# Kernel optimization log

Measured on AMD Instinct MI355X. Metric: run time of the kernel, lower is better.

Reference implementation:

```python
import jax, jax.numpy as jnp
import numpy as np
import math

D_MODEL = 1024
NUM_HEADS = 16
D_K = D_MODEL // NUM_HEADS
THETA = 10000.0
CONTEXT_LENGTH = 2048


def _rope_tables(seq_len):
    # freqs: [d_k/2]
    powers = jnp.arange(0, D_K, 2, dtype=jnp.float32) / D_K
    freqs = 1.0 / (THETA ** powers)
    t = jnp.arange(seq_len, dtype=jnp.float32)
    fm = jnp.outer(t, freqs)  # [s, d_k/2]
    return jnp.cos(fm), jnp.sin(fm)


def _apply_rope(x, cos, sin):
    # x: [b, h, s, d_k]; cos/sin: [s, d_k/2] broadcast to [1,1,s,d_k/2]
    c = cos[None, None, :, :].astype(x.dtype)
    s_ = sin[None, None, :, :].astype(x.dtype)
    xe = x[..., 0::2]
    xo = x[..., 1::2]
    oe = xe * c - xo * s_
    oo = xe * s_ + xo * c
    # interleave even/odd back
    out = jnp.stack([oe, oo], axis=-1).reshape(x.shape)
    return out


def setup_inputs() -> dict:
    key = jax.random.key(0)
    ks = jax.random.split(key, 5)
    b, s = 4, 2048
    std = (2.0 / (D_MODEL + D_MODEL)) ** 0.5
    x = jax.random.normal(ks[0], (b, s, D_MODEL), dtype=jnp.float32)
    Wq = jax.random.normal(ks[1], (D_MODEL, D_MODEL), dtype=jnp.float32) * std
    Wk = jax.random.normal(ks[2], (D_MODEL, D_MODEL), dtype=jnp.float32) * std
    Wv = jax.random.normal(ks[3], (D_MODEL, D_MODEL), dtype=jnp.float32) * std
    Wo = jax.random.normal(ks[4], (D_MODEL, D_MODEL), dtype=jnp.float32) * std
    return {"x": x, "Wq": Wq, "Wk": Wk, "Wv": Wv, "Wo": Wo}


def reference(x, Wq, Wk, Wv, Wo):
    b, s, d = x.shape
    h, dk = NUM_HEADS, D_K
    # projections: Linear applies x @ W.T via einsum('...i,oi->...o')
    def proj(W):
        y = jnp.einsum('bsi,oi->bso', x, W)
        return y.reshape(b, s, h, dk).transpose(0, 2, 1, 3)  # [b,h,s,dk]
    q, k, v = proj(Wq), proj(Wk), proj(Wv)
    cos, sin = _rope_tables(s)
    q = _apply_rope(q, cos, sin)
    k = _apply_rope(k, cos, sin)
    scores = jnp.einsum('bhnd,bhmd->bhnm', q, k) / math.sqrt(dk)
    causal = jnp.tril(jnp.ones((s, s), dtype=bool))
    scores = jnp.where(causal, scores, -jnp.inf)
    probs = jax.nn.softmax(scores, axis=-1)
    attn = jnp.einsum('bhnm,bhmd->bhnd', probs, v)
    attn = attn.transpose(0, 2, 1, 3).reshape(b, s, d)  # [b,s,d_model]
    return jnp.einsum('bsi,oi->bso', attn, Wo)
```

## Files before the change

### kernel.cpp

```cpp
#include <hip/hip_runtime.h>
#include <hip/hip_bf16.h>
#include <math.h>

typedef __attribute__((ext_vector_type(4))) float f32x4;
typedef __attribute__((ext_vector_type(8))) short s16x8;

#define LDSP(p) ((__attribute__((address_space(3))) void*)(p))
#define GLBP(p) ((const __attribute__((address_space(1))) void*)(p))

__device__ __forceinline__ unsigned short f2b(float f) {
  unsigned u = __builtin_bit_cast(unsigned, f);
  u += 0x7FFFu + ((u >> 16) & 1u);
  return (unsigned short)(u >> 16);
}
__device__ __forceinline__ float b2f(unsigned short h) {
  unsigned u = ((unsigned)h) << 16;
  return __builtin_bit_cast(float, u);
}

__global__ void cvt_f2b_kernel(const float* __restrict__ src, unsigned short* __restrict__ dst, int n8) {
  int i = blockIdx.x * blockDim.x + threadIdx.x;
  if (i >= n8) return;
  const float4* s = (const float4*)src;
  float4 a = s[2 * i], b = s[2 * i + 1];
  s16x8 o;
  o[0] = (short)f2b(a.x); o[1] = (short)f2b(a.y); o[2] = (short)f2b(a.z); o[3] = (short)f2b(a.w);
  o[4] = (short)f2b(b.x); o[5] = (short)f2b(b.y); o[6] = (short)f2b(b.z); o[7] = (short)f2b(b.w);
  ((s16x8*)dst)[i] = o;
}

__global__ void rope_table_kernel(float* __restrict__ cosT, float* __restrict__ sinT) {
  int idx = blockIdx.x * 256 + threadIdx.x;
  int s = idx >> 5, j = idx & 31;
  float freq = (float)(1.0 / pow(10000.0, (double)(2 * j) / 64.0));
  float fm = (float)s * freq;
  cosT[idx] = cosf(fm);
  sinT[idx] = sinf(fm);
}

__global__ void rope_apply_kernel(unsigned short* __restrict__ qk, const float* __restrict__ cosT,
                                  const float* __restrict__ sinT, float scale) {
  int i = blockIdx.x * 256 + threadIdx.x;
  int e = i * 8;
  int s = (e >> 6) & 2047;
  int jb = (e & 63) >> 1;
  s16x8 v = ((const s16x8*)qk)[i];
  float4 c = *(const float4*)(cosT + s * 32 + jb);
  float4 sn = *(const float4*)(sinT + s * 32 + jb);
  float cc[4] = {c.x, c.y, c.z, c.w}, ss[4] = {sn.x, sn.y, sn.z, sn.w};
  s16x8 o;
#pragma unroll
  for (int p = 0; p < 4; ++p) {
    float e_ = b2f((unsigned short)v[2 * p]);
    float o_ = b2f((unsigned short)v[2 * p + 1]);
    o[2 * p]     = (short)f2b((e_ * cc[p] - o_ * ss[p]) * scale);
    o[2 * p + 1] = (short)f2b((e_ * ss[p] + o_ * cc[p]) * scale);
  }
  ((s16x8*)qk)[i] = o;
}

template <int EPI>
__global__ void gemm_bt_kernel(const unsigned short* __restrict__ A, const unsigned short* __restrict__ B,
                               float* __restrict__ Cf, unsigned short* __restrict__ Cq,
                               unsigned short* __restrict__ Ck, unsigned short* __restrict__ Cv,
                               int M, int N, int K) {
  __shared__ __align__(16) unsigned short As[128 * 64];
  __shared__ __align__(16) unsigned short Bs[128 * 64];
  const int t = threadIdx.x;
  const int lane = t & 63, wave = t >> 6;
  const int wm = wave >> 1, wn = wave & 1;
  const int g = lane >> 4, q = lane & 15;
  const int m0 = blockIdx.x * 128, n0 = blockIdx.y * 128;
  const int srow = t >> 3;
  const int scol = (t & 7) << 4;
  f32x4 acc[4][4] = {};
  const int nkt = K >> 6;
  for (int kt = 0; kt < nkt; ++kt) {
    __syncthreads();
#pragma unroll
    for (int it = 0; it < 4; ++it) {
      int row = it * 32 + srow;
      int cg = scol ^ ((row & 7) << 4);
      const char* ga = (const char*)A + ((size_t)(m0 + row) * K + (kt << 6)) * 2 + cg;
      __builtin_amdgcn_global_load_lds(GLBP(ga), LDSP((char*)As + it * 4096 + wave * 1024), 16, 0, 0);
      const char* gb = (const char*)B + ((size_t)(n0 + row) * K + (kt << 6)) * 2 + cg;
      __builtin_amdgcn_global_load_lds(GLBP(gb), LDSP((char*)Bs + it * 4096 + wave * 1024), 16, 0, 0);
    }
    asm volatile("s_waitcnt vmcnt(0)" ::: "memory");
    __syncthreads();
#pragma unroll
    for (int kk = 0; kk < 2; ++kk) {
      const int colB = ((kk << 6) + (g << 4)) ^ ((q & 7) << 4);
      s16x8 af[4], bf[4];
#pragma unroll
      for (int x = 0; x < 4; ++x) {
        af[x] = *(const s16x8*)(As + (wm * 64 + x * 16 + q) * 64 + (colB >> 1));
        bf[x] = *(const s16x8*)(Bs + (wn * 64 + x * 16 + q) * 64 + (colB >> 1));
      }
#pragma unroll
      for (int mi = 0; mi < 4; ++mi)
#pragma unroll
        for (int ni = 0; ni < 4; ++ni)
          acc[mi][ni] = __builtin_amdgcn_mfma_f32_16x16x32_bf16(af[mi], bf[ni], acc[mi][ni], 0, 0, 0);
    }
  }
  if (EPI == 0) {
#pragma unroll
    for (int mi = 0; mi < 4; ++mi)
#pragma unroll
      for (int r = 0; r < 4; ++r) {
        int m = m0 + wm * 64 + mi * 16 + g * 4 + r;
#pragma unroll
        for (int ni = 0; ni < 4; ++ni) {
          int n = n0 + wn * 64 + ni * 16 + q;
          Cf[(size_t)m * N + n] = acc[mi][ni][r];
        }
      }
  } else {
    unsigned short* dst = (n0 < 1024) ? Cq : (n0 < 2048 ? Ck : Cv);
    const int obase = n0 & 1023;
#pragma unroll
    for (int mi = 0; mi < 4; ++mi)
#pragma unroll
      for (int r = 0; r < 4; ++r) {
        int m = m0 + wm * 64 + mi * 16 + g * 4 + r;
        int bb = m >> 11, s = m & 2047;
#pragma unroll
        for (int ni = 0; ni < 4; ++ni) {
          int o = obase + wn * 64 + ni * 16 + q;
          int hh = o >> 6, d = o & 63;
          dst[(((size_t)bb * 16 + hh) * 2048 + s) * 64 + d] = f2b(acc[mi][ni][r]);
        }
      }
  }
}

__global__ void attn_kernel(const unsigned short* __restrict__ Q, const unsigned short* __restrict__ K,
                            const unsigned short* __restrict__ V, unsigned short* __restrict__ O) {
  __shared__ __align__(16) unsigned short Ks[64 * 64];
  __shared__ __align__(16) unsigned short Vt[64 * 72];
  __shared__ __align__(16) unsigned short Ps[4 * 16 * 72];
  const int t = threadIdx.x;
  const int lane = t & 63, w = t >> 6;
  const int g = lane >> 4, q = lane & 15;
  const int bh = blockIdx.x;
  const int qt = 31 - (int)blockIdx.y;
  const size_t hoff = (size_t)bh * 2048 * 64;
  s16x8 qa[2];
  {
    const unsigned short* qp = Q + hoff + (size_t)(qt * 64 + w * 16 + q) * 64 + g * 8;
    qa[0] = *(const s16x8*)qp;
    qa[1] = *(const s16x8*)(qp + 32);
  }
  f32x4 accO[4] = {};
  float mrun[4] = {-3e38f, -3e38f, -3e38f, -3e38f};
  float lrun[4] = {0.f, 0.f, 0.f, 0.f};
  const int srow = t >> 3;
  const int scol = (t & 7) << 4;
  unsigned short* pw = Ps + w * (16 * 72);
  for (int tk = 0; tk <= qt; ++tk) {
    __syncthreads();
    const char* kb = (const char*)(K + hoff + (size_t)tk * 4096);
#pragma unroll
    for (int it = 0; it < 2; ++it) {
      int row = it * 32 + srow;
      int cg = scol ^ ((row & 7) << 4);
      __builtin_amdgcn_global_load_lds(GLBP(kb + row * 128 + cg), LDSP((char*)Ks + it * 4096 + w * 1024), 16, 0, 0);
    }
    {
      const unsigned short* vb = V + hoff + (size_t)tk * 4096;
#pragma unroll
      for (int p = 0; p < 2; ++p) {
        int d0 = w * 8 + p * 32;
        s16x8 vv = *(const s16x8*)(vb + lane * 64 + d0);
#pragma unroll
        for (int j = 0; j < 8; ++j) Vt[(d0 + j) * 72 + lane] = (unsigned short)vv[j];
      }
    }
    asm volatile("s_waitcnt vmcnt(0)" ::: "memory");
    __syncthreads();
    f32x4 accS[4] = {};
#pragma unroll
    for (int kk = 0; kk < 2; ++kk) {
      const int colB = ((kk << 6) + (g << 4)) ^ ((q & 7) << 4);
      s16x8 kf[4];
#pragma unroll
      for (int ni = 0; ni < 4; ++ni)
        kf[ni] = *(const s16x8*)(Ks + (ni * 16 + q) * 64 + (colB >> 1));
#pragma unroll
      for (int ni = 0; ni < 4; ++ni)
        accS[ni] = __builtin_amdgcn_mfma_f32_16x16x32_bf16(qa[kk], kf[ni], accS[ni], 0, 0, 0);
    }
    if (tk == qt) {
#pragma unroll
      for (int ni = 0; ni < 4; ++ni)
#pragma unroll
        for (int r = 0; r < 4; ++r) {
          int qrow = w * 16 + g * 4 + r;
          int kvc = ni * 16 + q;
          if (kvc > qrow) accS[ni][r] = -3e38f;
        }
    }
    float alph[4];
#pragma unroll
    for (int r = 0; r < 4; ++r) {
      float mx = fmaxf(fmaxf(accS[0][r], accS[1][r]), fmaxf(accS[2][r], accS[3][r]));
      mx = fmaxf(mx, __shfl_xor(mx, 1));
      mx = fmaxf(mx, __shfl_xor(mx, 2));
      mx = fmaxf(mx, __shfl_xor(mx, 4));
      mx = fmaxf(mx, __shfl_xor(mx, 8));
      float mnew = fmaxf(mrun[r], mx);
      float sum = 0.f;
#pragma unroll
      for (int ni = 0; ni < 4; ++ni) {
        float p = __expf(accS[ni][r] - mnew);
        accS[ni][r] = p;
        sum += p;
      }
      sum += __shfl_xor(sum, 1);
      sum += __shfl_xor(sum, 2);
      sum += __shfl_xor(sum, 4);
      sum += __shfl_xor(sum, 8);
      float alpha = __expf(mrun[r] - mnew);
      lrun[r] = lrun[r] * alpha + sum;
      mrun[r] = mnew;
      alph[r] = alpha;
    }
#pragma unroll
    for (int ni = 0; ni < 4; ++ni)
#pragma unroll
      for (int r = 0; r < 4; ++r) accO[ni][r] *= alph[r];
#pragma unroll
    for (int ni = 0; ni < 4; ++ni)
#pragma unroll
      for (int r = 0; r < 4; ++r)
        pw[(g * 4 + r) * 72 + ni * 16 + q] = f2b(accS[ni][r]);
#pragma unroll
    for (int kk = 0; kk < 2; ++kk) {
      s16x8 pa = *(const s16x8*)(pw + q * 72 + kk * 32 + g * 8);
#pragma unroll
      for (int ni = 0; ni < 4; ++ni) {
        s16x8 vf = *(const s16x8*)(Vt + (ni * 16 + q) * 72 + kk * 32 + g * 8);
        accO[ni] = __builtin_amdgcn_mfma_f32_16x16x32_bf16(pa, vf, accO[ni], 0, 0, 0);
      }
    }
  }
  const int bb = bh >> 4, hh = bh & 15;
#pragma unroll
  for (int ni = 0; ni < 4; ++ni)
#pragma unroll
    for (int r = 0; r < 4; ++r) {
      int s = qt * 64 + w * 16 + g * 4 + r;
      O[((size_t)(bb * 2048 + s)) * 1024 + hh * 64 + ni * 16 + q] = f2b(accO[ni][r] / lrun[r]);
    }
}

extern "C" void kernel_launch(void* const* d_in, const int* in_sizes, int n_in,
                              void* d_out, int out_size, void* d_ws, size_t ws_size,
                              hipStream_t stream) {
  const float* x  = (const float*)d_in[0];
  const float* Wq = (const float*)d_in[1];
  const float* Wk = (const float*)d_in[2];
  const float* Wv = (const float*)d_in[3];
  const float* Wo = (const float*)d_in[4];
  char* ws = (char*)d_ws;
  unsigned short* xb   = (unsigned short*)(ws);
  unsigned short* wqkv = (unsigned short*)(ws + 16777216);
  unsigned short* wo   = (unsigned short*)(ws + 23068672);
  unsigned short* qb   = (unsigned short*)(ws + 25165824);
  unsigned short* kb   = (unsigned short*)(ws + 41943040);
  unsigned short* vb   = (unsigned short*)(ws + 58720256);
  unsigned short* ab   = (unsigned short*)(ws + 75497472);
  float* cosT = (float*)(ws + 92274688);
  float* sinT = (float*)(ws + 92536832);

  cvt_f2b_kernel<<<4096, 256, 0, stream>>>(x, xb, 1048576);
  cvt_f2b_kernel<<<512, 256, 0, stream>>>(Wq, wqkv, 131072);
  cvt_f2b_kernel<<<512, 256, 0, stream>>>(Wk, wqkv + 1048576, 131072);
  cvt_f2b_kernel<<<512, 256, 0, stream>>>(Wv, wqkv + 2097152, 131072);
  cvt_f2b_kernel<<<512, 256, 0, stream>>>(Wo, wo, 131072);
  rope_table_kernel<<<256, 256, 0, stream>>>(cosT, sinT);
  gemm_bt_kernel<1><<<dim3(64, 24), 256, 0, stream>>>(xb, wqkv, nullptr, qb, kb, vb, 8192, 3072, 1024);
  rope_apply_kernel<<<4096, 256, 0, stream>>>(qb, cosT, sinT, 0.125f);
  rope_apply_kernel<<<4096, 256, 0, stream>>>(kb, cosT, sinT, 1.0f);
  attn_kernel<<<dim3(64, 32), 256, 0, stream>>>(qb, kb, vb, ab);
  gemm_bt_kernel<0><<<dim3(64, 8), 256, 0, stream>>>(ab, wo, (float*)d_out, nullptr, nullptr, nullptr, 8192, 1024, 1024);
}
```

Baseline: 304.4 us.

## Rewrite attention with 32x32 MFMA, 128-row query tiles, register-resident P

```diff
diff --git a/kernel.cpp b/kernel.cpp
--- a/kernel.cpp
+++ b/kernel.cpp
@@ -3,7 +3,9 @@
 #include <math.h>
 
 typedef __attribute__((ext_vector_type(4))) float f32x4;
+typedef __attribute__((ext_vector_type(16))) float f32x16;
 typedef __attribute__((ext_vector_type(8))) short s16x8;
+typedef __attribute__((ext_vector_type(4))) unsigned u32x4;
 
 #define LDSP(p) ((__attribute__((address_space(3))) void*)(p))
 #define GLBP(p) ((const __attribute__((address_space(1))) void*)(p))
@@ -16,6 +18,11 @@
 __device__ __forceinline__ float b2f(unsigned short h) {
   unsigned u = ((unsigned)h) << 16;
   return __builtin_bit_cast(float, u);
+}
+__device__ __forceinline__ unsigned cvtpk_bf16(float lo, float hi) {
+  unsigned r;
+  asm("v_cvt_pk_bf16_f32 %0, %1, %2" : "=v"(r) : "v"(lo), "v"(hi));
+  return r;
 }
 
 __global__ void cvt_f2b_kernel(const float* __restrict__ src, unsigned short* __restrict__ dst, int n8) {
@@ -135,124 +142,133 @@
   }
 }
 
+#define BUILD_PA(dst, SS, B) {                                        \
+    unsigned X  = cvtpk_bf16(SS[B + 0], SS[B + 1]);                   \
+    unsigned X2 = cvtpk_bf16(SS[B + 2], SS[B + 3]);                   \
+    unsigned Y  = cvtpk_bf16(SS[B + 4], SS[B + 5]);                   \
+    unsigned Y2 = cvtpk_bf16(SS[B + 6], SS[B + 7]);                   \
+    asm volatile("v_permlane32_swap_b32 %0, %1" : "+v"(X), "+v"(Y));  \
+    asm volatile("v_permlane32_swap_b32 %0, %1" : "+v"(X2), "+v"(Y2));\
+    u32x4 pw_; pw_[0] = X; pw_[1] = X2; pw_[2] = Y; pw_[3] = Y2;      \
+    dst = __builtin_bit_cast(s16x8, pw_); }
+
 __global__ void attn_kernel(const unsigned short* __restrict__ Q, const unsigned short* __restrict__ K,
                             const unsigned short* __restrict__ V, unsigned short* __restrict__ O) {
   __shared__ __align__(16) unsigned short Ks[64 * 64];
   __shared__ __align__(16) unsigned short Vt[64 * 72];
-  __shared__ __align__(16) unsigned short Ps[4 * 16 * 72];
   const int t = threadIdx.x;
   const int lane = t & 63, w = t >> 6;
-  const int g = lane >> 4, q = lane & 15;
+  const int h = lane >> 5, ql = lane & 31;
   const int bh = blockIdx.x;
-  const int qt = 31 - (int)blockIdx.y;
+  const int qt = 15 - (int)blockIdx.y;
   const size_t hoff = (size_t)bh * 2048 * 64;
-  s16x8 qa[2];
+  const int q_global = qt * 128 + w * 32 + ql;
+  const int qmax_w = qt * 128 + w * 32 + 31;
+
+  s16x8 qf[4];
   {
-    const unsigned short* qp = Q + hoff + (size_t)(qt * 64 + w * 16 + q) * 64 + g * 8;
-    qa[0] = *(const s16x8*)qp;
-    qa[1] = *(const s16x8*)(qp + 32);
-  }
-  f32x4 accO[4] = {};
-  float mrun[4] = {-3e38f, -3e38f, -3e38f, -3e38f};
-  float lrun[4] = {0.f, 0.f, 0.f, 0.f};
-  const int srow = t >> 3;
-  const int scol = (t & 7) << 4;
-  unsigned short* pw = Ps + w * (16 * 72);
-  for (int tk = 0; tk <= qt; ++tk) {
+    const unsigned short* qp = Q + hoff + (size_t)q_global * 64 + h * 8;
+#pragma unroll
+    for (int s = 0; s < 4; ++s) qf[s] = *(const s16x8*)(qp + 16 * s);
+  }
+  f32x16 accO[2] = {};
+  float mrun = -3e38f, lrun = 0.f;
+
+  const int srow = t >> 3, scol = (t & 7) << 4;
+  const int ntk = 2 * qt + 2;
+  for (int tk = 0; tk < ntk; ++tk) {
     __syncthreads();
-    const char* kb = (const char*)(K + hoff + (size_t)tk * 4096);
+    const char* kbp = (const char*)(K + hoff) + (size_t)tk * 8192;
 #pragma unroll
     for (int it = 0; it < 2; ++it) {
       int row = it * 32 + srow;
       int cg = scol ^ ((row & 7) << 4);
-      __builtin_amdgcn_global_load_lds(GLBP(kb + row * 128 + cg), LDSP((char*)Ks + it * 4096 + w * 1024), 16, 0, 0);
+      __builtin_amdgcn_global_load_lds(GLBP(kbp + row * 128 + cg),
+                                       LDSP((char*)Ks + it * 4096 + w * 1024), 16, 0, 0);
     }
     {
-      const unsigned short* vb = V + hoff + (size_t)tk * 4096;
+      const unsigned short* vbp = V + hoff + (size_t)tk * 4096;
 #pragma unroll
       for (int p = 0; p < 2; ++p) {
         int d0 = w * 8 + p * 32;
-        s16x8 vv = *(const s16x8*)(vb + lane * 64 + d0);
+        s16x8 vv = *(const s16x8*)(vbp + lane * 64 + d0);
 #pragma unroll
         for (int j = 0; j < 8; ++j) Vt[(d0 + j) * 72 + lane] = (unsigned short)vv[j];
       }
     }
     asm volatile("s_waitcnt vmcnt(0)" ::: "memory");
     __syncthreads();
-    f32x4 accS[4] = {};
-#pragma unroll
-    for (int kk = 0; kk < 2; ++kk) {
-      const int colB = ((kk << 6) + (g << 4)) ^ ((q & 7) << 4);
-      s16x8 kf[4];
-#pragma unroll
-      for (int ni = 0; ni < 4; ++ni)
-        kf[ni] = *(const s16x8*)(Ks + (ni * 16 + q) * 64 + (colB >> 1));
-#pragma unroll
-      for (int ni = 0; ni < 4; ++ni)
-        accS[ni] = __builtin_amdgcn_mfma_f32_16x16x32_bf16(qa[kk], kf[ni], accS[ni], 0, 0, 0);
-    }
-    if (tk == qt) {
-#pragma unroll
-      for (int ni = 0; ni < 4; ++ni)
-#pragma unroll
-        for (int r = 0; r < 4; ++r) {
-          int qrow = w * 16 + g * 4 + r;
-          int kvc = ni * 16 + q;
-          if (kvc > qrow) accS[ni][r] = -3e38f;
-        }
-    }
-    float alph[4];
-#pragma unroll
-    for (int r = 0; r < 4; ++r) {
-      float mx = fmaxf(fmaxf(accS[0][r], accS[1][r]), fmaxf(accS[2][r], accS[3][r]));
-      mx = fmaxf(mx, __shfl_xor(mx, 1));
-      mx = fmaxf(mx, __shfl_xor(mx, 2));
-      mx = fmaxf(mx, __shfl_xor(mx, 4));
-      mx = fmaxf(mx, __shfl_xor(mx, 8));
-      float mnew = fmaxf(mrun[r], mx);
-      float sum = 0.f;
-#pragma unroll
-      for (int ni = 0; ni < 4; ++ni) {
-        float p = __expf(accS[ni][r] - mnew);
-        accS[ni][r] = p;
-        sum += p;
-      }
-      sum += __shfl_xor(sum, 1);
-      sum += __shfl_xor(sum, 2);
-      sum += __shfl_xor(sum, 4);
-      sum += __shfl_xor(sum, 8);
-      float alpha = __expf(mrun[r] - mnew);
-      lrun[r] = lrun[r] * alpha + sum;
-      mrun[r] = mnew;
-      alph[r] = alpha;
-    }
-#pragma unroll
-    for (int ni = 0; ni < 4; ++ni)
-#pragma unroll
-      for (int r = 0; r < 4; ++r) accO[ni][r] *= alph[r];
-#pragma unroll
-    for (int ni = 0; ni < 4; ++ni)
-#pragma unroll
-      for (int r = 0; r < 4; ++r)
-        pw[(g * 4 + r) * 72 + ni * 16 + q] = f2b(accS[ni][r]);
-#pragma unroll
-    for (int kk = 0; kk < 2; ++kk) {
-      s16x8 pa = *(const s16x8*)(pw + q * 72 + kk * 32 + g * 8);
-#pragma unroll
-      for (int ni = 0; ni < 4; ++ni) {
-        s16x8 vf = *(const s16x8*)(Vt + (ni * 16 + q) * 72 + kk * 32 + g * 8);
-        accO[ni] = __builtin_amdgcn_mfma_f32_16x16x32_bf16(pa, vf, accO[ni], 0, 0, 0);
-      }
-    }
-  }
+    if (tk * 64 > qmax_w) continue;
+
+    f32x16 S0 = {}, S1 = {};
+#pragma unroll
+    for (int s = 0; s < 4; ++s) {
+      const int cb = 16 * h + 32 * s;
+      const int sw = (ql & 7) << 4;
+      s16x8 kf0 = *(const s16x8*)((const char*)Ks + ql * 128 + (cb ^ sw));
+      S0 = __builtin_amdgcn_mfma_f32_32x32x16_bf16(kf0, qf[s], S0, 0, 0, 0);
+      s16x8 kf1 = *(const s16x8*)((const char*)Ks + (32 + ql) * 128 + (cb ^ sw));
+      S1 = __builtin_amdgcn_mfma_f32_32x32x16_bf16(kf1, qf[s], S1, 0, 0, 0);
+    }
+    if (tk * 64 + 63 > qt * 128 + w * 32) {
+      const int kvb = tk * 64 + 4 * h;
+#pragma unroll
+      for (int r = 0; r < 16; ++r) {
+        const int kvl = (r & 3) + 8 * (r >> 2);
+        if (kvb + kvl > q_global) S0[r] = -3e38f;
+        if (kvb + 32 + kvl > q_global) S1[r] = -3e38f;
+      }
+    }
+    float pm = -3e38f;
+#pragma unroll
+    for (int r = 0; r < 16; ++r) pm = fmaxf(pm, fmaxf(S0[r], S1[r]));
+    pm = fmaxf(pm, __shfl_xor(pm, 32));
+    const float mnew = fmaxf(mrun, pm);
+    const float alpha = exp2f(mrun - mnew);
+    float ladd = 0.f;
+#pragma unroll
+    for (int r = 0; r < 16; ++r) {
+      float p0 = exp2f(S0[r] - mnew);
+      float p1 = exp2f(S1[r] - mnew);
+      S0[r] = p0; S1[r] = p1;
+      ladd += p0 + p1;
+    }
+    ladd += __shfl_xor(ladd, 32);
+    lrun = lrun * alpha + ladd;
+    mrun = mnew;
+    if (__any(alpha < 1.0f)) {
+#pragma unroll
+      for (int r = 0; r < 16; ++r) {
+        float ar = __shfl(alpha, 4 * h + (r & 3) + 8 * (r >> 2));
+        accO[0][r] *= ar;
+        accO[1][r] *= ar;
+      }
+    }
+    s16x8 pa[4];
+    BUILD_PA(pa[0], S0, 0);
+    BUILD_PA(pa[1], S0, 8);
+    BUILD_PA(pa[2], S1, 0);
+    BUILD_PA(pa[3], S1, 8);
+#pragma unroll
+    for (int s = 0; s < 4; ++s) {
+#pragma unroll
+      for (int dt = 0; dt < 2; ++dt) {
+        s16x8 vf = *(const s16x8*)(Vt + (dt * 32 + ql) * 72 + 8 * h + 16 * s);
+        accO[dt] = __builtin_amdgcn_mfma_f32_32x32x16_bf16(pa[s], vf, accO[dt], 0, 0, 0);
+      }
+    }
+  }
+  const float linv = 1.0f / lrun;
   const int bb = bh >> 4, hh = bh & 15;
 #pragma unroll
-  for (int ni = 0; ni < 4; ++ni)
-#pragma unroll
-    for (int r = 0; r < 4; ++r) {
-      int s = qt * 64 + w * 16 + g * 4 + r;
-      O[((size_t)(bb * 2048 + s)) * 1024 + hh * 64 + ni * 16 + q] = f2b(accO[ni][r] / lrun[r]);
-    }
+  for (int r = 0; r < 16; ++r) {
+    const int qrow = 4 * h + (r & 3) + 8 * (r >> 2);
+    const float lr = __shfl(linv, qrow);
+    const int sg = qt * 128 + w * 32 + qrow;
+    const size_t base = ((size_t)(bb * 2048 + sg)) * 1024 + hh * 64 + ql;
+    O[base] = f2b(accO[0][r] * lr);
+    O[base + 32] = f2b(accO[1][r] * lr);
+  }
 }
 
 extern "C" void kernel_launch(void* const* d_in, const int* in_sizes, int n_in,
@@ -281,8 +297,8 @@
   cvt_f2b_kernel<<<512, 256, 0, stream>>>(Wo, wo, 131072);
   rope_table_kernel<<<256, 256, 0, stream>>>(cosT, sinT);
   gemm_bt_kernel<1><<<dim3(64, 24), 256, 0, stream>>>(xb, wqkv, nullptr, qb, kb, vb, 8192, 3072, 1024);
-  rope_apply_kernel<<<4096, 256, 0, stream>>>(qb, cosT, sinT, 0.125f);
+  rope_apply_kernel<<<4096, 256, 0, stream>>>(qb, cosT, sinT, 0.125f * 1.44269504f);
   rope_apply_kernel<<<4096, 256, 0, stream>>>(kb, cosT, sinT, 1.0f);
-  attn_kernel<<<dim3(64, 32), 256, 0, stream>>>(qb, kb, vb, ab);
+  attn_kernel<<<dim3(64, 16), 256, 0, stream>>>(qb, kb, vb, ab);
   gemm_bt_kernel<0><<<dim3(64, 8), 256, 0, stream>>>(ab, wo, (float*)d_out, nullptr, nullptr, nullptr, 8192, 1024, 1024);
 }
```

Result: faster. 277.9 us (-8.7%).
